# Kernel tuning notes

Hardware: AMD Instinct MI355X
Metric: run time of the kernel (lower is better)

The kernel has to match this reference:

```python
import jax, jax.numpy as jnp
import numpy as np

N_NODES = 100000
N_EDGES = 1600000
IN_DIM = 64
HID_DIM = 64
NUM_CLASSES = 10
NUM_GRAPHS = 64


def setup_inputs() -> dict:
    key = jax.random.key(0)
    ks = jax.random.split(key, 8)
    x = jax.random.normal(ks[0], (N_NODES, IN_DIM), dtype=jnp.float32)
    edge_index = jax.random.randint(ks[1], (2, N_EDGES), 0, N_NODES, dtype=jnp.int32)
    batch = jnp.sort(jax.random.randint(ks[2], (N_NODES,), 0, NUM_GRAPHS, dtype=jnp.int32))
    # GCNConv weights (glorot-ish scale) and biases
    W1 = jax.random.normal(ks[3], (IN_DIM, HID_DIM), dtype=jnp.float32) / np.sqrt(IN_DIM)
    b1 = jnp.zeros((HID_DIM,), dtype=jnp.float32)
    W2 = jax.random.normal(ks[4], (HID_DIM, HID_DIM), dtype=jnp.float32) / np.sqrt(HID_DIM)
    b2 = jnp.zeros((HID_DIM,), dtype=jnp.float32)
    Wlin = jax.random.normal(ks[5], (HID_DIM, NUM_CLASSES), dtype=jnp.float32) / np.sqrt(HID_DIM)
    blin = jnp.zeros((NUM_CLASSES,), dtype=jnp.float32)
    return {"x": x, "edge_index": edge_index, "batch": batch,
            "W1": W1, "b1": b1, "W2": W2, "b2": b2, "Wlin": Wlin, "blin": blin}


def _gcn_conv(h, src, dst, norm, W, b, n_nodes):
    # h' = scatter_add( norm * (h W)[src] -> dst ) + b   (symmetric-normalized A+I)
    m = (h @ W)[src] * norm[:, None]          # [E+N, hid] edge messages (incl. self-loops)
    out = jax.ops.segment_sum(m, dst, num_segments=n_nodes)
    return out + b


def reference(x, edge_index, batch, W1, b1, W2, b2, Wlin, blin):
    n = x.shape[0]
    loops = jnp.arange(n, dtype=edge_index.dtype)
    src = jnp.concatenate([edge_index[0], loops])  # A + I self-loops
    dst = jnp.concatenate([edge_index[1], loops])
    deg = jax.ops.segment_sum(jnp.ones_like(dst, dtype=x.dtype), dst, num_segments=n)
    dinv = jax.lax.rsqrt(jnp.maximum(deg, 1.0))
    norm = dinv[src] * dinv[dst]               # D^{-1/2} (A+I) D^{-1/2} edge weights

    h = jax.nn.relu(_gcn_conv(x, src, dst, norm, W1, b1, n))
    h = jax.nn.relu(_gcn_conv(h, src, dst, norm, W2, b2, n))

    # global_mean_pool over batch segments
    sums = jax.ops.segment_sum(h, batch, num_segments=NUM_GRAPHS)
    cnts = jax.ops.segment_sum(jnp.ones((n,), dtype=h.dtype), batch, num_segments=NUM_GRAPHS)
    pooled = sums / jnp.maximum(cnts, 1.0)[:, None]
    return pooled @ Wlin + blin                # [G, num_classes]
```

## Files before the change

### kernel.cpp

```cpp
#include <hip/hip_runtime.h>
#include <hip/hip_bf16.h>


#define NDIM 64
#define NGRAPH 64
#define NREP 32
#define BSHIFT 7
#define BNODES 128
#define ECHUNK 8192

__device__ __forceinline__ unsigned short f32_to_bf16(float f) {
    unsigned int u = __float_as_uint(f);
    unsigned int r = 0x7FFFu + ((u >> 16) & 1u);
    return (unsigned short)((u + r) >> 16);
}

__global__ void bincnt_k(const int* __restrict__ dst, int* __restrict__ cntmat,
                         int e, int nb) {
    extern __shared__ int hist[];
    int t = threadIdx.x;
    for (int i = t; i < nb; i += 256) hist[i] = 0;
    __syncthreads();
    int base = blockIdx.x * ECHUNK + t;
#pragma unroll
    for (int k = 0; k < 32; ++k) {
        int i = base + k * 256;
        if (i < e) atomicAdd(&hist[dst[i] >> BSHIFT], 1);
    }
    __syncthreads();
    long row = (long)blockIdx.x * nb;
    for (int i = t; i < nb; i += 256) cntmat[row + i] = hist[i];
}

__global__ void colscan_k(const int* __restrict__ cntmat, int* __restrict__ basemat,
                          int* __restrict__ bucketTot, int nblk, int nb) {
    __shared__ int s[256];
    int b = blockIdx.x;
    int t = threadIdx.x;
    int v = (t < nblk) ? cntmat[(long)t * nb + b] : 0;
    s[t] = v;
    __syncthreads();
    for (int off = 1; off < 256; off <<= 1) {
        int tmp = (t >= off) ? s[t - off] : 0;
        __syncthreads();
        s[t] += tmp;
        __syncthreads();
    }
    if (t < nblk) basemat[(long)t * nb + b] = s[t] - v;
    if (t == 255) bucketTot[b] = s[255];
}

__global__ void bscan_k(const int* __restrict__ bucketTot, int* __restrict__ bucketStart,
                        int* __restrict__ start, int nb, int n, int e) {
    __shared__ int s[1024];
    int t = threadIdx.x;
    int v = (t < nb) ? bucketTot[t] : 0;
    s[t] = v;
    __syncthreads();
    for (int off = 1; off < 1024; off <<= 1) {
        int tmp = (t >= off) ? s[t - off] : 0;
        __syncthreads();
        s[t] += tmp;
        __syncthreads();
    }
    if (t < nb) bucketStart[t + 1] = s[t];
    if (t == 0) { bucketStart[0] = 0; start[n] = e; }
}

__global__ void bscatter_k(const int* __restrict__ src, const int* __restrict__ dst,
                           const int* __restrict__ bucketStart,
                           const int* __restrict__ basemat,
                           unsigned int* __restrict__ ebuf, int e, int nb) {
    extern __shared__ int cur[];
    int t = threadIdx.x;
    long row = (long)blockIdx.x * nb;
    for (int i = t; i < nb; i += 256) cur[i] = bucketStart[i] + basemat[row + i];
    __syncthreads();
    int base = blockIdx.x * ECHUNK + t;
#pragma unroll
    for (int k = 0; k < 32; ++k) {
        int i = base + k * 256;
        if (i < e) {
            int d = dst[i];
            int b = d >> BSHIFT;
            int pos = atomicAdd(&cur[b], 1);
            ebuf[pos] = ((unsigned)(d & (BNODES - 1)) << 25) | (unsigned)src[i];
        }
    }
}

__global__ void fill2_k(const unsigned int* __restrict__ ebuf,
                        const int* __restrict__ bucketStart,
                        const int* __restrict__ batch, float* __restrict__ dinv,
                        int* __restrict__ start, int* __restrict__ csr,
                        int* __restrict__ gstart, int* __restrict__ gend, int n) {
    __shared__ int scnt[BNODES], sincl[BNODES], scur[BNODES];
    int t = threadIdx.x;
    int b = blockIdx.x;
    int node0 = b << BSHIFT;
    int nNodes = min(BNODES, n - node0);
    if (t < BNODES) scnt[t] = 0;
    int e0 = bucketStart[b], e1 = bucketStart[b + 1];
    __syncthreads();
    for (int i = e0 + t; i < e1; i += 256)
        atomicAdd(&scnt[ebuf[i] >> 25], 1);
    __syncthreads();
    int val = (t < BNODES) ? scnt[t] : 0;
    if (t < BNODES) sincl[t] = val;
    __syncthreads();
    for (int off = 1; off < BNODES; off <<= 1) {
        int tmp = (t >= off && t < BNODES) ? sincl[t - off] : 0;
        __syncthreads();
        if (t < BNODES) sincl[t] += tmp;
        __syncthreads();
    }
    if (t < nNodes) {
        int v = node0 + t;
        int st = e0 + sincl[t] - val;
        start[v] = st;
        scur[t] = st;
        dinv[v] = rsqrtf((float)(val + 1));
        int g = batch[v];
        if (v == 0 || batch[v - 1] != g) gstart[g] = v;
        if (v == n - 1 || batch[v + 1] != g) gend[g] = v + 1;
    }
    __syncthreads();
    for (int i = e0 + t; i < e1; i += 256) {
        unsigned rec = ebuf[i];
        int pos = atomicAdd(&scur[rec >> 25], 1);
        csr[pos] = (int)(rec & 0x1FFFFFFu);
    }
}

__global__ void gemm_k(const float* __restrict__ A, const float* __restrict__ W,
                       const float* __restrict__ scale,
                       unsigned long long* __restrict__ C, int n) {
    __shared__ float4 Wl4[64 * 16];
    __shared__ float4 Xl4[64 * 16];
    int t = threadIdx.x;
    const float4* W4 = (const float4*)W;
#pragma unroll
    for (int i = 0; i < 4; ++i) Wl4[t + 256 * i] = W4[t + 256 * i];
    const float4* A4 = (const float4*)A;
    long fbase = (long)blockIdx.x * 1024;
    long fmax  = (long)n * 16;
#pragma unroll
    for (int i = 0; i < 4; ++i) {
        long f = fbase + t + 256 * i;
        float4 v;
        if (f < fmax) v = A4[f];
        else { v.x = 0.f; v.y = 0.f; v.z = 0.f; v.w = 0.f; }
        Xl4[t + 256 * i] = v;
    }
    __syncthreads();
    int rg = t >> 4, cg = t & 15;
    float a00 = 0.f, a01 = 0.f, a02 = 0.f, a03 = 0.f;
    float a10 = 0.f, a11 = 0.f, a12 = 0.f, a13 = 0.f;
    float a20 = 0.f, a21 = 0.f, a22 = 0.f, a23 = 0.f;
    float a30 = 0.f, a31 = 0.f, a32 = 0.f, a33 = 0.f;
#pragma unroll 4
    for (int k4 = 0; k4 < 16; ++k4) {
        float4 w0 = Wl4[(4 * k4 + 0) * 16 + cg];
        float4 w1 = Wl4[(4 * k4 + 1) * 16 + cg];
        float4 w2 = Wl4[(4 * k4 + 2) * 16 + cg];
        float4 w3 = Wl4[(4 * k4 + 3) * 16 + cg];
        float4 x0 = Xl4[(4 * rg + 0) * 16 + k4];
        float4 x1 = Xl4[(4 * rg + 1) * 16 + k4];
        float4 x2 = Xl4[(4 * rg + 2) * 16 + k4];
        float4 x3 = Xl4[(4 * rg + 3) * 16 + k4];
        a00 += x0.x * w0.x + x0.y * w1.x + x0.z * w2.x + x0.w * w3.x;
        a01 += x0.x * w0.y + x0.y * w1.y + x0.z * w2.y + x0.w * w3.y;
        a02 += x0.x * w0.z + x0.y * w1.z + x0.z * w2.z + x0.w * w3.z;
        a03 += x0.x * w0.w + x0.y * w1.w + x0.z * w2.w + x0.w * w3.w;
        a10 += x1.x * w0.x + x1.y * w1.x + x1.z * w2.x + x1.w * w3.x;
        a11 += x1.x * w0.y + x1.y * w1.y + x1.z * w2.y + x1.w * w3.y;
        a12 += x1.x * w0.z + x1.y * w1.z + x1.z * w2.z + x1.w * w3.z;
        a13 += x1.x * w0.w + x1.y * w1.w + x1.z * w2.w + x1.w * w3.w;
        a20 += x2.x * w0.x + x2.y * w1.x + x2.z * w2.x + x2.w * w3.x;
        a21 += x2.x * w0.y + x2.y * w1.y + x2.z * w2.y + x2.w * w3.y;
        a22 += x2.x * w0.z + x2.y * w1.z + x2.z * w2.z + x2.w * w3.z;
        a23 += x2.x * w0.w + x2.y * w1.w + x2.z * w2.w + x2.w * w3.w;
        a30 += x3.x * w0.x + x3.y * w1.x + x3.z * w2.x + x3.w * w3.x;
        a31 += x3.x * w0.y + x3.y * w1.y + x3.z * w2.y + x3.w * w3.y;
        a32 += x3.x * w0.z + x3.y * w1.z + x3.z * w2.z + x3.w * w3.z;
        a33 += x3.x * w0.w + x3.y * w1.w + x3.z * w2.w + x3.w * w3.w;
    }
    int vb = blockIdx.x * 64 + rg * 4;
    int v;
    float s;
    unsigned long long u;
    v = vb + 0;
    if (v < n) {
        s = scale[v];
        u  = (unsigned long long)(((unsigned int)f32_to_bf16(s * a01) << 16) | (unsigned int)f32_to_bf16(s * a00));
        u |= (unsigned long long)(((unsigned int)f32_to_bf16(s * a03) << 16) | (unsigned int)f32_to_bf16(s * a02)) << 32;
        C[(long)v * 16 + cg] = u;
    }
    v = vb + 1;
    if (v < n) {
        s = scale[v];
        u  = (unsigned long long)(((unsigned int)f32_to_bf16(s * a11) << 16) | (unsigned int)f32_to_bf16(s * a10));
        u |= (unsigned long long)(((unsigned int)f32_to_bf16(s * a13) << 16) | (unsigned int)f32_to_bf16(s * a12)) << 32;
        C[(long)v * 16 + cg] = u;
    }
    v = vb + 2;
    if (v < n) {
        s = scale[v];
        u  = (unsigned long long)(((unsigned int)f32_to_bf16(s * a21) << 16) | (unsigned int)f32_to_bf16(s * a20));
        u |= (unsigned long long)(((unsigned int)f32_to_bf16(s * a23) << 16) | (unsigned int)f32_to_bf16(s * a22)) << 32;
        C[(long)v * 16 + cg] = u;
    }
    v = vb + 3;
    if (v < n) {
        s = scale[v];
        u  = (unsigned long long)(((unsigned int)f32_to_bf16(s * a31) << 16) | (unsigned int)f32_to_bf16(s * a30));
        u |= (unsigned long long)(((unsigned int)f32_to_bf16(s * a33) << 16) | (unsigned int)f32_to_bf16(s * a32)) << 32;
        C[(long)v * 16 + cg] = u;
    }
}

__device__ __forceinline__ float gather_row(const unsigned int* __restrict__ xp,
                                            const int* __restrict__ csr,
                                            int s0, int d0, int h, int p, int v) {
    float l0 = 0.f, l1 = 0.f, l2 = 0.f, l3 = 0.f;
    float h0 = 0.f, h1 = 0.f, h2 = 0.f, h3 = 0.f;
    int i = 0;
    for (; i + 16 <= d0; i += 16) {
        int j0 = csr[s0 + i +  0 + h];
        int j1 = csr[s0 + i +  2 + h];
        int j2 = csr[s0 + i +  4 + h];
        int j3 = csr[s0 + i +  6 + h];
        int j4 = csr[s0 + i +  8 + h];
        int j5 = csr[s0 + i + 10 + h];
        int j6 = csr[s0 + i + 12 + h];
        int j7 = csr[s0 + i + 14 + h];
        unsigned int u0 = xp[(long)j0 * 32 + p];
        unsigned int u1 = xp[(long)j1 * 32 + p];
        unsigned int u2 = xp[(long)j2 * 32 + p];
        unsigned int u3 = xp[(long)j3 * 32 + p];
        unsigned int u4 = xp[(long)j4 * 32 + p];
        unsigned int u5 = xp[(long)j5 * 32 + p];
        unsigned int u6 = xp[(long)j6 * 32 + p];
        unsigned int u7 = xp[(long)j7 * 32 + p];
        l0 += __uint_as_float(u0 << 16);  h0 += __uint_as_float(u0 & 0xFFFF0000u);
        l1 += __uint_as_float(u1 << 16);  h1 += __uint_as_float(u1 & 0xFFFF0000u);
        l2 += __uint_as_float(u2 << 16);  h2 += __uint_as_float(u2 & 0xFFFF0000u);
        l3 += __uint_as_float(u3 << 16);  h3 += __uint_as_float(u3 & 0xFFFF0000u);
        l0 += __uint_as_float(u4 << 16);  h0 += __uint_as_float(u4 & 0xFFFF0000u);
        l1 += __uint_as_float(u5 << 16);  h1 += __uint_as_float(u5 & 0xFFFF0000u);
        l2 += __uint_as_float(u6 << 16);  h2 += __uint_as_float(u6 & 0xFFFF0000u);
        l3 += __uint_as_float(u7 << 16);  h3 += __uint_as_float(u7 & 0xFFFF0000u);
    }
    for (; i + 8 <= d0; i += 8) {
        int j0 = csr[s0 + i + 0 + h];
        int j1 = csr[s0 + i + 2 + h];
        int j2 = csr[s0 + i + 4 + h];
        int j3 = csr[s0 + i + 6 + h];
        unsigned int u0 = xp[(long)j0 * 32 + p];
        unsigned int u1 = xp[(long)j1 * 32 + p];
        unsigned int u2 = xp[(long)j2 * 32 + p];
        unsigned int u3 = xp[(long)j3 * 32 + p];
        l0 += __uint_as_float(u0 << 16);  h0 += __uint_as_float(u0 & 0xFFFF0000u);
        l1 += __uint_as_float(u1 << 16);  h1 += __uint_as_float(u1 & 0xFFFF0000u);
        l2 += __uint_as_float(u2 << 16);  h2 += __uint_as_float(u2 & 0xFFFF0000u);
        l3 += __uint_as_float(u3 << 16);  h3 += __uint_as_float(u3 & 0xFFFF0000u);
    }
    for (; i + 4 <= d0; i += 4) {
        int j0 = csr[s0 + i + 0 + h];
        int j1 = csr[s0 + i + 2 + h];
        unsigned int u0 = xp[(long)j0 * 32 + p];
        unsigned int u1 = xp[(long)j1 * 32 + p];
        l0 += __uint_as_float(u0 << 16);  h0 += __uint_as_float(u0 & 0xFFFF0000u);
        l1 += __uint_as_float(u1 << 16);  h1 += __uint_as_float(u1 & 0xFFFF0000u);
    }
    for (; i + 2 <= d0; i += 2) {
        int j = csr[s0 + i + h];
        unsigned int u = xp[(long)j * 32 + p];
        l0 += __uint_as_float(u << 16);
        h0 += __uint_as_float(u & 0xFFFF0000u);
    }
    if (i < d0 && h == 0) {
        int j = csr[s0 + i];
        unsigned int u = xp[(long)j * 32 + p];
        l0 += __uint_as_float(u << 16);
        h0 += __uint_as_float(u & 0xFFFF0000u);
    }
    float al = (l0 + l1) + (l2 + l3);
    float ah = (h0 + h1) + (h2 + h3);
    al += __shfl_xor(al, 32);
    ah += __shfl_xor(ah, 32);
    unsigned int us = xp[(long)v * 32 + p];
    al += __uint_as_float(us << 16);
    ah += __uint_as_float(us & 0xFFFF0000u);
    return h ? ah : al;
}

__global__ void agg_k(const unsigned int* __restrict__ xp, const float* __restrict__ dinv,
                      const int* __restrict__ start, const int* __restrict__ csr,
                      const float* __restrict__ bias, float* __restrict__ out, int n) {
    int t = threadIdx.x;
    int lane = t & 63;
    int h = lane >> 5;
    int p = lane & 31;
    int v = blockIdx.x * 4 + (t >> 6);
    if (v >= n) return;
    int s0 = start[v];
    int d0 = start[v + 1] - s0;
    float sum = gather_row(xp, csr, s0, d0, h, p, v);
    int d = 2 * p + h;
    float val = sum * dinv[v] + bias[d];
    out[(long)v * NDIM + d] = fmaxf(val, 0.f);
}

__global__ void aggpool_k(const unsigned int* __restrict__ xp, const float* __restrict__ dinv,
                          const int* __restrict__ start, const int* __restrict__ csr,
                          const float* __restrict__ b2, const int* __restrict__ batch,
                          float* __restrict__ pooledR, int n) {
    int t = threadIdx.x;
    int lane = t & 63;
    int h = lane >> 5, p = lane & 31;
    int wid = blockIdx.x * 4 + (t >> 6);
    int v0 = wid * 4;
    if (v0 >= n) return;
    int v1 = min(v0 + 4, n);
    int d = 2 * p + h;
    float bias = b2[d];
    long rbase = (long)(wid & (NREP - 1)) * (NGRAPH * NDIM);
    int gcur = -1;
    float acc = 0.f;
    for (int v = v0; v < v1; ++v) {
        int g = batch[v];
        if (g != gcur) {
            if (gcur >= 0) atomicAdd(&pooledR[rbase + gcur * NDIM + d], acc);
            gcur = g;
            acc = 0.f;
        }
        int s0 = start[v];
        int d0 = start[v + 1] - s0;
        float sum = gather_row(xp, csr, s0, d0, h, p, v);
        acc += fmaxf(sum * dinv[v] + bias, 0.f);
    }
    if (gcur >= 0) atomicAdd(&pooledR[rbase + gcur * NDIM + d], acc);
}

__global__ void reduce_k(const float* __restrict__ pooledR, float* __restrict__ pooled) {
    int t = blockIdx.x * 256 + threadIdx.x;
    if (t >= NGRAPH * NDIM) return;
    float s = 0.f;
    for (int r = 0; r < NREP; ++r) s += pooledR[(long)r * (NGRAPH * NDIM) + t];
    pooled[t] = s;
}

__global__ void final_k(const float* __restrict__ pooled, const int* __restrict__ gstart,
                        const int* __restrict__ gend,
                        const float* __restrict__ Wlin, const float* __restrict__ blin,
                        float* __restrict__ out, int nclass) {
    int t = blockIdx.x * blockDim.x + threadIdx.x;
    if (t >= NGRAPH * nclass) return;
    int g = t / nclass, c = t % nclass;
    float cnt = (float)(gend[g] - gstart[g]);
    float inv = 1.f / fmaxf(cnt, 1.f);
    float acc = 0.f;
    for (int j = 0; j < NDIM; ++j) acc += pooled[g * NDIM + j] * Wlin[j * nclass + c];
    out[t] = acc * inv + blin[c];
}

extern "C" void kernel_launch(void* const* d_in, const int* in_sizes, int n_in,
                              void* d_out, int out_size, void* d_ws, size_t ws_size,
                              hipStream_t stream) {
    const float* x     = (const float*)d_in[0];
    const int*   ei    = (const int*)d_in[1];
    const int*   batch = (const int*)d_in[2];
    const float* W1    = (const float*)d_in[3];
    const float* b1    = (const float*)d_in[4];
    const float* W2    = (const float*)d_in[5];
    const float* b2    = (const float*)d_in[6];
    const float* Wlin  = (const float*)d_in[7];
    const float* blin  = (const float*)d_in[8];
    float* out = (float*)d_out;

    const int N = in_sizes[0] / NDIM;
    const int E = in_sizes[1] / 2;
    const int NCLASS = in_sizes[7] / NDIM;
    const int* src = ei;
    const int* dst = ei + E;
    const int NB   = (N + BNODES - 1) >> BSHIFT;
    const int NBLK = (E + ECHUNK - 1) / ECHUNK;

    size_t o = 0;
    char* wsp = (char*)d_ws;
    auto take = [&](size_t nbytes) -> void* {
        void* p = (void*)(wsp + o);
        o += (nbytes + 255) & ~(size_t)255;
        return p;
    };
    int*   gstart    = (int*)take(NGRAPH * 4);
    int*   gend      = (int*)take(NGRAPH * 4);
    float* pooledR   = (float*)take((size_t)NREP * NGRAPH * NDIM * 4);
    size_t zero_bytes = o;
    float* pooled    = (float*)take(NGRAPH * NDIM * 4);
    int*   cntmat   = (int*)take((size_t)NBLK * NB * 4);
    int*   basemat  = (int*)take((size_t)NBLK * NB * 4);
    int*   bucketTot   = (int*)take((size_t)NB * 4);
    int*   bucketStart = (int*)take((size_t)(NB + 1) * 4);
    float* dinv  = (float*)take((size_t)N * 4);
    int*   start = (int*)take((size_t)(N + 1) * 4);
    int*   csr   = (int*)take((size_t)E * 4);
    unsigned int* ebuf = (unsigned int*)take((size_t)E * 4);
    unsigned int* xws  = (unsigned int*)take((size_t)N * NDIM * 2);
    float* h     = (float*)take((size_t)N * NDIM * 4);
    (void)ws_size;

    hipMemsetAsync(d_ws, 0, zero_bytes, stream);

    int rbl = (N + 3) / 4;
    int gbl = (N + 63) / 64;
    int pbl = (N + 15) / 16;

    bincnt_k<<<NBLK, 256, (size_t)NB * 4, stream>>>(dst, cntmat, E, NB);
    colscan_k<<<NB, 256, 0, stream>>>(cntmat, basemat, bucketTot, NBLK, NB);
    bscan_k<<<1, 1024, 0, stream>>>(bucketTot, bucketStart, start, NB, N, E);
    bscatter_k<<<NBLK, 256, (size_t)NB * 4, stream>>>(src, dst, bucketStart, basemat, ebuf, E, NB);
    fill2_k<<<NB, 256, 0, stream>>>(ebuf, bucketStart, batch, dinv, start, csr, gstart, gend, N);

    gemm_k<<<gbl, 256, 0, stream>>>(x, W1, dinv, (unsigned long long*)xws, N);
    agg_k<<<rbl, 256, 0, stream>>>(xws, dinv, start, csr, b1, h, N);
    gemm_k<<<gbl, 256, 0, stream>>>(h, W2, dinv, (unsigned long long*)xws, N);
    aggpool_k<<<pbl, 256, 0, stream>>>(xws, dinv, start, csr, b2, batch, pooledR, N);
    reduce_k<<<(NGRAPH * NDIM + 255) / 256, 256, 0, stream>>>(pooledR, pooled);
    final_k<<<(NGRAPH * NCLASS + 255) / 256, 256, 0, stream>>>(pooled, gstart, gend, Wlin, blin, out, NCLASS);
}
```

Baseline: 279.9 us.

## Pad CSR rows to multiples of four with self-loop and dummy node

```diff
diff --git a/kernel.cpp b/kernel.cpp
--- a/kernel.cpp
+++ b/kernel.cpp
@@ -7,7 +7,11 @@
 #define NREP 32
 #define BSHIFT 7
 #define BNODES 128
+#define PADSLOT (BNODES * 4)
 #define ECHUNK 8192
+
+#define BLO(u) __uint_as_float((u) << 16)
+#define BHI(u) __uint_as_float((u) & 0xFFFF0000u)
 
 __device__ __forceinline__ unsigned short f32_to_bf16(float f) {
     unsigned int u = __float_as_uint(f);
@@ -92,7 +96,8 @@
 __global__ void fill2_k(const unsigned int* __restrict__ ebuf,
                         const int* __restrict__ bucketStart,
                         const int* __restrict__ batch, float* __restrict__ dinv,
-                        int* __restrict__ start, int* __restrict__ csr,
+                        int* __restrict__ start, int* __restrict__ m4,
+                        int* __restrict__ csr,
                         int* __restrict__ gstart, int* __restrict__ gend, int n) {
     __shared__ int scnt[BNODES], sincl[BNODES], scur[BNODES];
     int t = threadIdx.x;
@@ -106,7 +111,8 @@
         atomicAdd(&scnt[ebuf[i] >> 25], 1);
     __syncthreads();
     int val = (t < BNODES) ? scnt[t] : 0;
-    if (t < BNODES) sincl[t] = val;
+    int slots = (t < nNodes) ? ((val + 4) & ~3) : 0;
+    if (t < BNODES) sincl[t] = slots;
     __syncthreads();
     for (int off = 1; off < BNODES; off <<= 1) {
         int tmp = (t >= off && t < BNODES) ? sincl[t - off] : 0;
@@ -116,10 +122,13 @@
     }
     if (t < nNodes) {
         int v = node0 + t;
-        int st = e0 + sincl[t] - val;
+        int st = e0 + b * PADSLOT + sincl[t] - slots;
         start[v] = st;
+        m4[v] = slots >> 2;
         scur[t] = st;
         dinv[v] = rsqrtf((float)(val + 1));
+        csr[st + val] = v;
+        for (int k2 = val + 1; k2 < slots; ++k2) csr[st + k2] = n;
         int g = batch[v];
         if (v == 0 || batch[v - 1] != g) gstart[g] = v;
         if (v == n - 1 || batch[v + 1] != g) gend[g] = v + 1;
@@ -219,128 +228,138 @@
     }
 }
 
-__device__ __forceinline__ float gather_row(const unsigned int* __restrict__ xp,
-                                            const int* __restrict__ csr,
-                                            int s0, int d0, int h, int p, int v) {
-    float l0 = 0.f, l1 = 0.f, l2 = 0.f, l3 = 0.f;
-    float h0 = 0.f, h1 = 0.f, h2 = 0.f, h3 = 0.f;
-    int i = 0;
-    for (; i + 16 <= d0; i += 16) {
-        int j0 = csr[s0 + i +  0 + h];
-        int j1 = csr[s0 + i +  2 + h];
-        int j2 = csr[s0 + i +  4 + h];
-        int j3 = csr[s0 + i +  6 + h];
-        int j4 = csr[s0 + i +  8 + h];
-        int j5 = csr[s0 + i + 10 + h];
-        int j6 = csr[s0 + i + 12 + h];
-        int j7 = csr[s0 + i + 14 + h];
-        unsigned int u0 = xp[(long)j0 * 32 + p];
-        unsigned int u1 = xp[(long)j1 * 32 + p];
-        unsigned int u2 = xp[(long)j2 * 32 + p];
-        unsigned int u3 = xp[(long)j3 * 32 + p];
-        unsigned int u4 = xp[(long)j4 * 32 + p];
-        unsigned int u5 = xp[(long)j5 * 32 + p];
-        unsigned int u6 = xp[(long)j6 * 32 + p];
-        unsigned int u7 = xp[(long)j7 * 32 + p];
-        l0 += __uint_as_float(u0 << 16);  h0 += __uint_as_float(u0 & 0xFFFF0000u);
-        l1 += __uint_as_float(u1 << 16);  h1 += __uint_as_float(u1 & 0xFFFF0000u);
-        l2 += __uint_as_float(u2 << 16);  h2 += __uint_as_float(u2 & 0xFFFF0000u);
-        l3 += __uint_as_float(u3 << 16);  h3 += __uint_as_float(u3 & 0xFFFF0000u);
-        l0 += __uint_as_float(u4 << 16);  h0 += __uint_as_float(u4 & 0xFFFF0000u);
-        l1 += __uint_as_float(u5 << 16);  h1 += __uint_as_float(u5 & 0xFFFF0000u);
-        l2 += __uint_as_float(u6 << 16);  h2 += __uint_as_float(u6 & 0xFFFF0000u);
-        l3 += __uint_as_float(u7 << 16);  h3 += __uint_as_float(u7 & 0xFFFF0000u);
-    }
-    for (; i + 8 <= d0; i += 8) {
-        int j0 = csr[s0 + i + 0 + h];
-        int j1 = csr[s0 + i + 2 + h];
-        int j2 = csr[s0 + i + 4 + h];
-        int j3 = csr[s0 + i + 6 + h];
-        unsigned int u0 = xp[(long)j0 * 32 + p];
-        unsigned int u1 = xp[(long)j1 * 32 + p];
-        unsigned int u2 = xp[(long)j2 * 32 + p];
-        unsigned int u3 = xp[(long)j3 * 32 + p];
-        l0 += __uint_as_float(u0 << 16);  h0 += __uint_as_float(u0 & 0xFFFF0000u);
-        l1 += __uint_as_float(u1 << 16);  h1 += __uint_as_float(u1 & 0xFFFF0000u);
-        l2 += __uint_as_float(u2 << 16);  h2 += __uint_as_float(u2 & 0xFFFF0000u);
-        l3 += __uint_as_float(u3 << 16);  h3 += __uint_as_float(u3 & 0xFFFF0000u);
-    }
-    for (; i + 4 <= d0; i += 4) {
-        int j0 = csr[s0 + i + 0 + h];
-        int j1 = csr[s0 + i + 2 + h];
-        unsigned int u0 = xp[(long)j0 * 32 + p];
-        unsigned int u1 = xp[(long)j1 * 32 + p];
-        l0 += __uint_as_float(u0 << 16);  h0 += __uint_as_float(u0 & 0xFFFF0000u);
-        l1 += __uint_as_float(u1 << 16);  h1 += __uint_as_float(u1 & 0xFFFF0000u);
-    }
-    for (; i + 2 <= d0; i += 2) {
-        int j = csr[s0 + i + h];
-        unsigned int u = xp[(long)j * 32 + p];
-        l0 += __uint_as_float(u << 16);
-        h0 += __uint_as_float(u & 0xFFFF0000u);
-    }
-    if (i < d0 && h == 0) {
-        int j = csr[s0 + i];
-        unsigned int u = xp[(long)j * 32 + p];
-        l0 += __uint_as_float(u << 16);
-        h0 += __uint_as_float(u & 0xFFFF0000u);
-    }
-    float al = (l0 + l1) + (l2 + l3);
-    float ah = (h0 + h1) + (h2 + h3);
-    al += __shfl_xor(al, 32);
-    ah += __shfl_xor(ah, 32);
-    unsigned int us = xp[(long)v * 32 + p];
-    al += __uint_as_float(us << 16);
-    ah += __uint_as_float(us & 0xFFFF0000u);
-    return h ? ah : al;
+__device__ __forceinline__ void gather4(const unsigned int* __restrict__ xp,
+                                        const int* __restrict__ csr,
+                                        int s0, int m, int q, int r,
+                                        float& o0, float& o1, float& o2, float& o3) {
+    const uint2* __restrict__ xp2 = (const uint2*)xp;
+    float a0 = 0.f, a1 = 0.f, a2 = 0.f, a3 = 0.f;
+    float b0 = 0.f, b1 = 0.f, b2 = 0.f, b3 = 0.f;
+    int c = s0 + q;
+    while (m >= 8) {
+        int j0 = csr[c +  0];
+        int j1 = csr[c +  4];
+        int j2 = csr[c +  8];
+        int j3 = csr[c + 12];
+        int j4 = csr[c + 16];
+        int j5 = csr[c + 20];
+        int j6 = csr[c + 24];
+        int j7 = csr[c + 28];
+        uint2 u0 = xp2[((unsigned)j0 << 4) + r];
+        uint2 u1 = xp2[((unsigned)j1 << 4) + r];
+        uint2 u2 = xp2[((unsigned)j2 << 4) + r];
+        uint2 u3 = xp2[((unsigned)j3 << 4) + r];
+        uint2 u4 = xp2[((unsigned)j4 << 4) + r];
+        uint2 u5 = xp2[((unsigned)j5 << 4) + r];
+        uint2 u6 = xp2[((unsigned)j6 << 4) + r];
+        uint2 u7 = xp2[((unsigned)j7 << 4) + r];
+        a0 += BLO(u0.x); a1 += BHI(u0.x); a2 += BLO(u0.y); a3 += BHI(u0.y);
+        b0 += BLO(u1.x); b1 += BHI(u1.x); b2 += BLO(u1.y); b3 += BHI(u1.y);
+        a0 += BLO(u2.x); a1 += BHI(u2.x); a2 += BLO(u2.y); a3 += BHI(u2.y);
+        b0 += BLO(u3.x); b1 += BHI(u3.x); b2 += BLO(u3.y); b3 += BHI(u3.y);
+        a0 += BLO(u4.x); a1 += BHI(u4.x); a2 += BLO(u4.y); a3 += BHI(u4.y);
+        b0 += BLO(u5.x); b1 += BHI(u5.x); b2 += BLO(u5.y); b3 += BHI(u5.y);
+        a0 += BLO(u6.x); a1 += BHI(u6.x); a2 += BLO(u6.y); a3 += BHI(u6.y);
+        b0 += BLO(u7.x); b1 += BHI(u7.x); b2 += BLO(u7.y); b3 += BHI(u7.y);
+        c += 32; m -= 8;
+    }
+    if (m > 0) {
+        int j0, j1, j2, j3, j4, j5, j6;
+        uint2 u0, u1, u2, u3, u4, u5, u6;
+        j0 = csr[c];
+        if (m > 1) j1 = csr[c +  4];
+        if (m > 2) j2 = csr[c +  8];
+        if (m > 3) j3 = csr[c + 12];
+        if (m > 4) j4 = csr[c + 16];
+        if (m > 5) j5 = csr[c + 20];
+        if (m > 6) j6 = csr[c + 24];
+        u0 = xp2[((unsigned)j0 << 4) + r];
+        if (m > 1) u1 = xp2[((unsigned)j1 << 4) + r];
+        if (m > 2) u2 = xp2[((unsigned)j2 << 4) + r];
+        if (m > 3) u3 = xp2[((unsigned)j3 << 4) + r];
+        if (m > 4) u4 = xp2[((unsigned)j4 << 4) + r];
+        if (m > 5) u5 = xp2[((unsigned)j5 << 4) + r];
+        if (m > 6) u6 = xp2[((unsigned)j6 << 4) + r];
+        a0 += BLO(u0.x); a1 += BHI(u0.x); a2 += BLO(u0.y); a3 += BHI(u0.y);
+        if (m > 1) { b0 += BLO(u1.x); b1 += BHI(u1.x); b2 += BLO(u1.y); b3 += BHI(u1.y); }
+        if (m > 2) { a0 += BLO(u2.x); a1 += BHI(u2.x); a2 += BLO(u2.y); a3 += BHI(u2.y); }
+        if (m > 3) { b0 += BLO(u3.x); b1 += BHI(u3.x); b2 += BLO(u3.y); b3 += BHI(u3.y); }
+        if (m > 4) { a0 += BLO(u4.x); a1 += BHI(u4.x); a2 += BLO(u4.y); a3 += BHI(u4.y); }
+        if (m > 5) { b0 += BLO(u5.x); b1 += BHI(u5.x); b2 += BLO(u5.y); b3 += BHI(u5.y); }
+        if (m > 6) { a0 += BLO(u6.x); a1 += BHI(u6.x); a2 += BLO(u6.y); a3 += BHI(u6.y); }
+    }
+    a0 += b0; a1 += b1; a2 += b2; a3 += b3;
+    a0 += __shfl_xor(a0, 16); a0 += __shfl_xor(a0, 32);
+    a1 += __shfl_xor(a1, 16); a1 += __shfl_xor(a1, 32);
+    a2 += __shfl_xor(a2, 16); a2 += __shfl_xor(a2, 32);
+    a3 += __shfl_xor(a3, 16); a3 += __shfl_xor(a3, 32);
+    o0 = a0; o1 = a1; o2 = a2; o3 = a3;
 }
 
 __global__ void agg_k(const unsigned int* __restrict__ xp, const float* __restrict__ dinv,
-                      const int* __restrict__ start, const int* __restrict__ csr,
-                      const float* __restrict__ bias, float* __restrict__ out, int n) {
+                      const int* __restrict__ start, const int* __restrict__ m4,
+                      const int* __restrict__ csr, const float* __restrict__ bias,
+                      float* __restrict__ out, int n) {
     int t = threadIdx.x;
     int lane = t & 63;
-    int h = lane >> 5;
-    int p = lane & 31;
+    int q = lane >> 4, r = lane & 15;
     int v = blockIdx.x * 4 + (t >> 6);
     if (v >= n) return;
-    int s0 = start[v];
-    int d0 = start[v + 1] - s0;
-    float sum = gather_row(xp, csr, s0, d0, h, p, v);
-    int d = 2 * p + h;
-    float val = sum * dinv[v] + bias[d];
-    out[(long)v * NDIM + d] = fmaxf(val, 0.f);
+    int s0 = start[v], m = m4[v];
+    float g0, g1, g2, g3;
+    gather4(xp, csr, s0, m, q, r, g0, g1, g2, g3);
+    float dv = dinv[v];
+    float4 bb = ((const float4*)bias)[r];
+    float4 o;
+    o.x = fmaxf(fmaf(g0, dv, bb.x), 0.f);
+    o.y = fmaxf(fmaf(g1, dv, bb.y), 0.f);
+    o.z = fmaxf(fmaf(g2, dv, bb.z), 0.f);
+    o.w = fmaxf(fmaf(g3, dv, bb.w), 0.f);
+    if (q == 0) ((float4*)out)[(long)v * 16 + r] = o;
 }
 
 __global__ void aggpool_k(const unsigned int* __restrict__ xp, const float* __restrict__ dinv,
-                          const int* __restrict__ start, const int* __restrict__ csr,
-                          const float* __restrict__ b2, const int* __restrict__ batch,
-                          float* __restrict__ pooledR, int n) {
+                          const int* __restrict__ start, const int* __restrict__ m4,
+                          const int* __restrict__ csr, const float* __restrict__ b2,
+                          const int* __restrict__ batch, float* __restrict__ pooledR, int n) {
     int t = threadIdx.x;
     int lane = t & 63;
-    int h = lane >> 5, p = lane & 31;
+    int q = lane >> 4, r = lane & 15;
     int wid = blockIdx.x * 4 + (t >> 6);
     int v0 = wid * 4;
     if (v0 >= n) return;
     int v1 = min(v0 + 4, n);
-    int d = 2 * p + h;
-    float bias = b2[d];
+    float4 bb = ((const float4*)b2)[r];
     long rbase = (long)(wid & (NREP - 1)) * (NGRAPH * NDIM);
     int gcur = -1;
-    float acc = 0.f;
+    float p0 = 0.f, p1 = 0.f, p2 = 0.f, p3 = 0.f;
     for (int v = v0; v < v1; ++v) {
         int g = batch[v];
         if (g != gcur) {
-            if (gcur >= 0) atomicAdd(&pooledR[rbase + gcur * NDIM + d], acc);
+            if (gcur >= 0 && q == 0) {
+                atomicAdd(&pooledR[rbase + gcur * NDIM + 4 * r + 0], p0);
+                atomicAdd(&pooledR[rbase + gcur * NDIM + 4 * r + 1], p1);
+                atomicAdd(&pooledR[rbase + gcur * NDIM + 4 * r + 2], p2);
+                atomicAdd(&pooledR[rbase + gcur * NDIM + 4 * r + 3], p3);
+            }
             gcur = g;
-            acc = 0.f;
+            p0 = p1 = p2 = p3 = 0.f;
         }
-        int s0 = start[v];
-        int d0 = start[v + 1] - s0;
-        float sum = gather_row(xp, csr, s0, d0, h, p, v);
-        acc += fmaxf(sum * dinv[v] + bias, 0.f);
-    }
-    if (gcur >= 0) atomicAdd(&pooledR[rbase + gcur * NDIM + d], acc);
+        int s0 = start[v], m = m4[v];
+        float g0, g1, g2, g3;
+        gather4(xp, csr, s0, m, q, r, g0, g1, g2, g3);
+        float dv = dinv[v];
+        p0 += fmaxf(fmaf(g0, dv, bb.x), 0.f);
+        p1 += fmaxf(fmaf(g1, dv, bb.y), 0.f);
+        p2 += fmaxf(fmaf(g2, dv, bb.z), 0.f);
+        p3 += fmaxf(fmaf(g3, dv, bb.w), 0.f);
+    }
+    if (gcur >= 0 && q == 0) {
+        atomicAdd(&pooledR[rbase + gcur * NDIM + 4 * r + 0], p0);
+        atomicAdd(&pooledR[rbase + gcur * NDIM + 4 * r + 1], p1);
+        atomicAdd(&pooledR[rbase + gcur * NDIM + 4 * r + 2], p2);
+        atomicAdd(&pooledR[rbase + gcur * NDIM + 4 * r + 3], p3);
+    }
 }
 
 __global__ void reduce_k(const float* __restrict__ pooledR, float* __restrict__ pooled) {
@@ -405,13 +424,15 @@
     int*   bucketStart = (int*)take((size_t)(NB + 1) * 4);
     float* dinv  = (float*)take((size_t)N * 4);
     int*   start = (int*)take((size_t)(N + 1) * 4);
-    int*   csr   = (int*)take((size_t)E * 4);
+    int*   m4    = (int*)take((size_t)N * 4);
+    int*   csr   = (int*)take(((size_t)E + (size_t)NB * PADSLOT + 64) * 4);
     unsigned int* ebuf = (unsigned int*)take((size_t)E * 4);
-    unsigned int* xws  = (unsigned int*)take((size_t)N * NDIM * 2);
+    unsigned int* xws  = (unsigned int*)take((size_t)(N + 1) * NDIM * 2);
     float* h     = (float*)take((size_t)N * NDIM * 4);
     (void)ws_size;
 
     hipMemsetAsync(d_ws, 0, zero_bytes, stream);
+    hipMemsetAsync((char*)xws + (size_t)N * NDIM * 2, 0, NDIM * 2, stream);
 
     int rbl = (N + 3) / 4;
     int gbl = (N + 63) / 64;
@@ -421,12 +442,12 @@
     colscan_k<<<NB, 256, 0, stream>>>(cntmat, basemat, bucketTot, NBLK, NB);
     bscan_k<<<1, 1024, 0, stream>>>(bucketTot, bucketStart, start, NB, N, E);
     bscatter_k<<<NBLK, 256, (size_t)NB * 4, stream>>>(src, dst, bucketStart, basemat, ebuf, E, NB);
-    fill2_k<<<NB, 256, 0, stream>>>(ebuf, bucketStart, batch, dinv, start, csr, gstart, gend, N);
+    fill2_k<<<NB, 256, 0, stream>>>(ebuf, bucketStart, batch, dinv, start, m4, csr, gstart, gend, N);
 
     gemm_k<<<gbl, 256, 0, stream>>>(x, W1, dinv, (unsigned long long*)xws, N);
-    agg_k<<<rbl, 256, 0, stream>>>(xws, dinv, start, csr, b1, h, N);
+    agg_k<<<rbl, 256, 0, stream>>>(xws, dinv, start, m4, csr, b1, h, N);
     gemm_k<<<gbl, 256, 0, stream>>>(h, W2, dinv, (unsigned long long*)xws, N);
-    aggpool_k<<<pbl, 256, 0, stream>>>(xws, dinv, start, csr, b2, batch, pooledR, N);
+    aggpool_k<<<pbl, 256, 0, stream>>>(xws, dinv, start, m4, csr, b2, batch, pooledR, N);
     reduce_k<<<(NGRAPH * NDIM + 255) / 256, 256, 0, stream>>>(pooledR, pooled);
     final_k<<<(NGRAPH * NCLASS + 255) / 256, 256, 0, stream>>>(pooled, gstart, gend, Wlin, blin, out, NCLASS);
 }
```

New measurement: 322.7 us. +15.3%, slower.

## Pad CSR rows to multiples of 16 with self-loop and dummy zero node

Applied to the files above, without the earlier changes.

```diff
diff --git a/kernel.cpp b/kernel.cpp
--- a/kernel.cpp
+++ b/kernel.cpp
@@ -7,7 +7,11 @@
 #define NREP 32
 #define BSHIFT 7
 #define BNODES 128
+#define PADSLOT (BNODES * 16)
 #define ECHUNK 8192
+
+#define BLO(u) __uint_as_float((u) << 16)
+#define BHI(u) __uint_as_float((u) & 0xFFFF0000u)
 
 __device__ __forceinline__ unsigned short f32_to_bf16(float f) {
     unsigned int u = __float_as_uint(f);
@@ -92,7 +96,8 @@
 __global__ void fill2_k(const unsigned int* __restrict__ ebuf,
                         const int* __restrict__ bucketStart,
                         const int* __restrict__ batch, float* __restrict__ dinv,
-                        int* __restrict__ start, int* __restrict__ csr,
+                        int* __restrict__ start, int* __restrict__ m16,
+                        int* __restrict__ csr,
                         int* __restrict__ gstart, int* __restrict__ gend, int n) {
     __shared__ int scnt[BNODES], sincl[BNODES], scur[BNODES];
     int t = threadIdx.x;
@@ -106,7 +111,8 @@
         atomicAdd(&scnt[ebuf[i] >> 25], 1);
     __syncthreads();
     int val = (t < BNODES) ? scnt[t] : 0;
-    if (t < BNODES) sincl[t] = val;
+    int slots = (t < nNodes) ? ((val + 16) & ~15) : 0;
+    if (t < BNODES) sincl[t] = slots;
     __syncthreads();
     for (int off = 1; off < BNODES; off <<= 1) {
         int tmp = (t >= off && t < BNODES) ? sincl[t - off] : 0;
@@ -116,10 +122,13 @@
     }
     if (t < nNodes) {
         int v = node0 + t;
-        int st = e0 + sincl[t] - val;
+        int st = e0 + b * PADSLOT + sincl[t] - slots;
         start[v] = st;
+        m16[v] = slots >> 4;
         scur[t] = st;
         dinv[v] = rsqrtf((float)(val + 1));
+        csr[st + val] = v;
+        for (int k2 = val + 1; k2 < slots; ++k2) csr[st + k2] = n;
         int g = batch[v];
         if (v == 0 || batch[v - 1] != g) gstart[g] = v;
         if (v == n - 1 || batch[v + 1] != g) gend[g] = v + 1;
@@ -219,21 +228,21 @@
     }
 }
 
-__device__ __forceinline__ float gather_row(const unsigned int* __restrict__ xp,
-                                            const int* __restrict__ csr,
-                                            int s0, int d0, int h, int p, int v) {
+__device__ __forceinline__ float gather_p(const unsigned int* __restrict__ xp,
+                                          const int* __restrict__ csr,
+                                          int s0, int m16, int h, int p) {
     float l0 = 0.f, l1 = 0.f, l2 = 0.f, l3 = 0.f;
     float h0 = 0.f, h1 = 0.f, h2 = 0.f, h3 = 0.f;
-    int i = 0;
-    for (; i + 16 <= d0; i += 16) {
-        int j0 = csr[s0 + i +  0 + h];
-        int j1 = csr[s0 + i +  2 + h];
-        int j2 = csr[s0 + i +  4 + h];
-        int j3 = csr[s0 + i +  6 + h];
-        int j4 = csr[s0 + i +  8 + h];
-        int j5 = csr[s0 + i + 10 + h];
-        int j6 = csr[s0 + i + 12 + h];
-        int j7 = csr[s0 + i + 14 + h];
+    int c = s0 + h;
+    for (int it = 0; it < m16; ++it) {
+        int j0 = csr[c +  0];
+        int j1 = csr[c +  2];
+        int j2 = csr[c +  4];
+        int j3 = csr[c +  6];
+        int j4 = csr[c +  8];
+        int j5 = csr[c + 10];
+        int j6 = csr[c + 12];
+        int j7 = csr[c + 14];
         unsigned int u0 = xp[(long)j0 * 32 + p];
         unsigned int u1 = xp[(long)j1 * 32 + p];
         unsigned int u2 = xp[(long)j2 * 32 + p];
@@ -242,80 +251,43 @@
         unsigned int u5 = xp[(long)j5 * 32 + p];
         unsigned int u6 = xp[(long)j6 * 32 + p];
         unsigned int u7 = xp[(long)j7 * 32 + p];
-        l0 += __uint_as_float(u0 << 16);  h0 += __uint_as_float(u0 & 0xFFFF0000u);
-        l1 += __uint_as_float(u1 << 16);  h1 += __uint_as_float(u1 & 0xFFFF0000u);
-        l2 += __uint_as_float(u2 << 16);  h2 += __uint_as_float(u2 & 0xFFFF0000u);
-        l3 += __uint_as_float(u3 << 16);  h3 += __uint_as_float(u3 & 0xFFFF0000u);
-        l0 += __uint_as_float(u4 << 16);  h0 += __uint_as_float(u4 & 0xFFFF0000u);
-        l1 += __uint_as_float(u5 << 16);  h1 += __uint_as_float(u5 & 0xFFFF0000u);
-        l2 += __uint_as_float(u6 << 16);  h2 += __uint_as_float(u6 & 0xFFFF0000u);
-        l3 += __uint_as_float(u7 << 16);  h3 += __uint_as_float(u7 & 0xFFFF0000u);
-    }
-    for (; i + 8 <= d0; i += 8) {
-        int j0 = csr[s0 + i + 0 + h];
-        int j1 = csr[s0 + i + 2 + h];
-        int j2 = csr[s0 + i + 4 + h];
-        int j3 = csr[s0 + i + 6 + h];
-        unsigned int u0 = xp[(long)j0 * 32 + p];
-        unsigned int u1 = xp[(long)j1 * 32 + p];
-        unsigned int u2 = xp[(long)j2 * 32 + p];
-        unsigned int u3 = xp[(long)j3 * 32 + p];
-        l0 += __uint_as_float(u0 << 16);  h0 += __uint_as_float(u0 & 0xFFFF0000u);
-        l1 += __uint_as_float(u1 << 16);  h1 += __uint_as_float(u1 & 0xFFFF0000u);
-        l2 += __uint_as_float(u2 << 16);  h2 += __uint_as_float(u2 & 0xFFFF0000u);
-        l3 += __uint_as_float(u3 << 16);  h3 += __uint_as_float(u3 & 0xFFFF0000u);
-    }
-    for (; i + 4 <= d0; i += 4) {
-        int j0 = csr[s0 + i + 0 + h];
-        int j1 = csr[s0 + i + 2 + h];
-        unsigned int u0 = xp[(long)j0 * 32 + p];
-        unsigned int u1 = xp[(long)j1 * 32 + p];
-        l0 += __uint_as_float(u0 << 16);  h0 += __uint_as_float(u0 & 0xFFFF0000u);
-        l1 += __uint_as_float(u1 << 16);  h1 += __uint_as_float(u1 & 0xFFFF0000u);
-    }
-    for (; i + 2 <= d0; i += 2) {
-        int j = csr[s0 + i + h];
-        unsigned int u = xp[(long)j * 32 + p];
-        l0 += __uint_as_float(u << 16);
-        h0 += __uint_as_float(u & 0xFFFF0000u);
-    }
-    if (i < d0 && h == 0) {
-        int j = csr[s0 + i];
-        unsigned int u = xp[(long)j * 32 + p];
-        l0 += __uint_as_float(u << 16);
-        h0 += __uint_as_float(u & 0xFFFF0000u);
+        l0 += BLO(u0);  h0 += BHI(u0);
+        l1 += BLO(u1);  h1 += BHI(u1);
+        l2 += BLO(u2);  h2 += BHI(u2);
+        l3 += BLO(u3);  h3 += BHI(u3);
+        l0 += BLO(u4);  h0 += BHI(u4);
+        l1 += BLO(u5);  h1 += BHI(u5);
+        l2 += BLO(u6);  h2 += BHI(u6);
+        l3 += BLO(u7);  h3 += BHI(u7);
+        c += 16;
     }
     float al = (l0 + l1) + (l2 + l3);
     float ah = (h0 + h1) + (h2 + h3);
     al += __shfl_xor(al, 32);
     ah += __shfl_xor(ah, 32);
-    unsigned int us = xp[(long)v * 32 + p];
-    al += __uint_as_float(us << 16);
-    ah += __uint_as_float(us & 0xFFFF0000u);
     return h ? ah : al;
 }
 
 __global__ void agg_k(const unsigned int* __restrict__ xp, const float* __restrict__ dinv,
-                      const int* __restrict__ start, const int* __restrict__ csr,
-                      const float* __restrict__ bias, float* __restrict__ out, int n) {
+                      const int* __restrict__ start, const int* __restrict__ m16,
+                      const int* __restrict__ csr, const float* __restrict__ bias,
+                      float* __restrict__ out, int n) {
     int t = threadIdx.x;
     int lane = t & 63;
     int h = lane >> 5;
     int p = lane & 31;
     int v = blockIdx.x * 4 + (t >> 6);
     if (v >= n) return;
-    int s0 = start[v];
-    int d0 = start[v + 1] - s0;
-    float sum = gather_row(xp, csr, s0, d0, h, p, v);
+    float sum = gather_p(xp, csr, start[v], m16[v], h, p);
     int d = 2 * p + h;
     float val = sum * dinv[v] + bias[d];
     out[(long)v * NDIM + d] = fmaxf(val, 0.f);
 }
 
 __global__ void aggpool_k(const unsigned int* __restrict__ xp, const float* __restrict__ dinv,
-                          const int* __restrict__ start, const int* __restrict__ csr,
-                          const float* __restrict__ b2, const int* __restrict__ batch,
-                          float* __restrict__ pooledR, int n) {
+                          const int* __restrict__ start, const int* __restrict__ m16,
+                          const int* __restrict__ csr, const float* __restrict__ b2,
+                          const int* __restrict__ batch, float* __restrict__ pooledR, int n) {
     int t = threadIdx.x;
     int lane = t & 63;
     int h = lane >> 5, p = lane & 31;
@@ -335,9 +307,7 @@
             gcur = g;
             acc = 0.f;
         }
-        int s0 = start[v];
-        int d0 = start[v + 1] - s0;
-        float sum = gather_row(xp, csr, s0, d0, h, p, v);
+        float sum = gather_p(xp, csr, start[v], m16[v], h, p);
         acc += fmaxf(sum * dinv[v] + bias, 0.f);
     }
     if (gcur >= 0) atomicAdd(&pooledR[rbase + gcur * NDIM + d], acc);
@@ -405,13 +375,15 @@
     int*   bucketStart = (int*)take((size_t)(NB + 1) * 4);
     float* dinv  = (float*)take((size_t)N * 4);
     int*   start = (int*)take((size_t)(N + 1) * 4);
-    int*   csr   = (int*)take((size_t)E * 4);
-    unsigned int* ebuf = (unsigned int*)take((size_t)E * 4);
-    unsigned int* xws  = (unsigned int*)take((size_t)N * NDIM * 2);
+    int*   m16   = (int*)take((size_t)N * 4);
+    int*   csr   = (int*)take(((size_t)E + (size_t)NB * PADSLOT + 64) * 4);
+    unsigned int* xws  = (unsigned int*)take((size_t)(N + 1) * NDIM * 2);
     float* h     = (float*)take((size_t)N * NDIM * 4);
+    unsigned int* ebuf = (unsigned int*)h;
     (void)ws_size;
 
     hipMemsetAsync(d_ws, 0, zero_bytes, stream);
+    hipMemsetAsync((char*)xws + (size_t)N * NDIM * 2, 0, NDIM * 2, stream);
 
     int rbl = (N + 3) / 4;
     int gbl = (N + 63) / 64;
@@ -421,12 +393,12 @@
     colscan_k<<<NB, 256, 0, stream>>>(cntmat, basemat, bucketTot, NBLK, NB);
     bscan_k<<<1, 1024, 0, stream>>>(bucketTot, bucketStart, start, NB, N, E);
     bscatter_k<<<NBLK, 256, (size_t)NB * 4, stream>>>(src, dst, bucketStart, basemat, ebuf, E, NB);
-    fill2_k<<<NB, 256, 0, stream>>>(ebuf, bucketStart, batch, dinv, start, csr, gstart, gend, N);
+    fill2_k<<<NB, 256, 0, stream>>>(ebuf, bucketStart, batch, dinv, start, m16, csr, gstart, gend, N);
 
     gemm_k<<<gbl, 256, 0, stream>>>(x, W1, dinv, (unsigned long long*)xws, N);
-    agg_k<<<rbl, 256, 0, stream>>>(xws, dinv, start, csr, b1, h, N);
+    agg_k<<<rbl, 256, 0, stream>>>(xws, dinv, start, m16, csr, b1, h, N);
     gemm_k<<<gbl, 256, 0, stream>>>(h, W2, dinv, (unsigned long long*)xws, N);
-    aggpool_k<<<pbl, 256, 0, stream>>>(xws, dinv, start, csr, b2, batch, pooledR, N);
+    aggpool_k<<<pbl, 256, 0, stream>>>(xws, dinv, start, m16, csr, b2, batch, pooledR, N);
     reduce_k<<<(NGRAPH * NDIM + 255) / 256, 256, 0, stream>>>(pooledR, pooled);
     final_k<<<(NGRAPH * NCLASS + 255) / 256, 256, 0, stream>>>(pooled, gstart, gend, Wlin, blin, out, NCLASS);
 }
```

Result: no change. 276.6 us (-1.2%).
